# Kernel tuning notes

Measured on AMD Instinct MI355X. Metric: run time of the kernel, lower is better.

## Reference

```python
import jax, jax.numpy as jnp
import numpy as np


def _pair_indices(field_num):
    # upper-triangular (row < col) pairs, same order as the torch double loop
    r, c = np.triu_indices(field_num, k=1)
    return jnp.asarray(r, dtype=jnp.int32), jnp.asarray(c, dtype=jnp.int32)


def setup_inputs() -> dict:
    key = jax.random.key(0)
    x = jax.random.normal(key, (4096, 39, 64), dtype=jnp.float32)
    return {"x": x}


def reference(x) -> jnp.ndarray:
    # x: (B, F, D). Output: (B, F*(F-1)/2) pairwise inner products.
    field_num = x.shape[1]
    rows, cols = _pair_indices(field_num)  # static: derived from shape
    p = x[:, rows, :]  # (B, P, D) gather of row-field embeddings
    q = x[:, cols, :]  # (B, P, D) gather of col-field embeddings
    return jnp.sum(p * q, axis=2)  # (B, P)
```

## Files before the change

### kernel.cpp

```cpp
#include <hip/hip_runtime.h>


typedef __bf16 bf16x8 __attribute__((ext_vector_type(8)));
typedef float  f32x4  __attribute__((ext_vector_type(4)));

constexpr int NFIELD = 39;
constexpr int DIM    = 64;
constexpr int NPAIR  = 741;
constexpr int BPB    = 4;

__global__ __launch_bounds__(256)
void ip_kernel(const float* __restrict__ x, float* __restrict__ out, int batches) {
    __shared__ __align__(16) float lds_out[BPB][NPAIR];

    const int tid  = threadIdx.x;
    const int wv   = tid >> 6;
    const int lane = tid & 63;
    const int b0   = blockIdx.x * BPB;
    const int batch = b0 + wv;
    const int nb_here = (batches - b0) < BPB ? (batches - b0) : BPB;

    if (batch < batches) {
        const int m = lane & 15;
        const int q = lane >> 4;
        const float* xb = x + (size_t)batch * (NFIELD * DIM);

        bf16x8 fr[3][2];
        #pragma unroll
        for (int t = 0; t < 3; ++t) {
            int row = 16 * t + m;
            if (row >= NFIELD) row = NFIELD - 1;
            #pragma unroll
            for (int s = 0; s < 2; ++s) {
                const float* p = xb + row * DIM + 32 * s + 8 * q;
                f32x4 u = *(const f32x4*)p;
                f32x4 v = *(const f32x4*)(p + 4);
                bf16x8 w;
                w[0] = (__bf16)u[0]; w[1] = (__bf16)u[1];
                w[2] = (__bf16)u[2]; w[3] = (__bf16)u[3];
                w[4] = (__bf16)v[0]; w[5] = (__bf16)v[1];
                w[6] = (__bf16)v[2]; w[7] = (__bf16)v[3];
                fr[t][s] = w;
            }
        }

        f32x4 a00 = {0.f,0.f,0.f,0.f}, a01 = a00, a02 = a00;
        f32x4 a11 = a00, a12 = a00, a22 = a00;
        #pragma unroll
        for (int s = 0; s < 2; ++s) {
            a00 = __builtin_amdgcn_mfma_f32_16x16x32_bf16(fr[0][s], fr[0][s], a00, 0, 0, 0);
            a01 = __builtin_amdgcn_mfma_f32_16x16x32_bf16(fr[0][s], fr[1][s], a01, 0, 0, 0);
            a02 = __builtin_amdgcn_mfma_f32_16x16x32_bf16(fr[0][s], fr[2][s], a02, 0, 0, 0);
            a11 = __builtin_amdgcn_mfma_f32_16x16x32_bf16(fr[1][s], fr[1][s], a11, 0, 0, 0);
            a12 = __builtin_amdgcn_mfma_f32_16x16x32_bf16(fr[1][s], fr[2][s], a12, 0, 0, 0);
            a22 = __builtin_amdgcn_mfma_f32_16x16x32_bf16(fr[2][s], fr[2][s], a22, 0, 0, 0);
        }

        auto scatter = [&](const f32x4& a, int ti, int tj) {
            #pragma unroll
            for (int r = 0; r < 4; ++r) {
                const int i = 16 * ti + 4 * q + r;
                const int j = 16 * tj + m;
                if (i < j && j < NFIELD) {
                    const int p = 38 * i - (i * (i - 1)) / 2 + (j - i - 1);
                    lds_out[wv][p] = a[r];
                }
            }
        };
        scatter(a00, 0, 0); scatter(a01, 0, 1); scatter(a02, 0, 2);
        scatter(a11, 1, 1); scatter(a12, 1, 2); scatter(a22, 2, 2);
    }
    __syncthreads();

    float* dst = out + (size_t)b0 * NPAIR;
    const float* srcf = &lds_out[0][0];
    if (nb_here == BPB) {
        const float4* s4 = (const float4*)srcf;
        float4* d4 = (float4*)dst;
        for (int i = tid; i < (BPB * NPAIR) / 4; i += 256) d4[i] = s4[i];
    } else {
        const int nfl = nb_here * NPAIR;
        for (int i = tid; i < nfl; i += 256) dst[i] = srcf[i];
    }
}

extern "C" void kernel_launch(void* const* d_in, const int* in_sizes, int n_in,
                              void* d_out, int out_size, void* d_ws, size_t ws_size,
                              hipStream_t stream) {
    const float* x = (const float*)d_in[0];
    float* out     = (float*)d_out;
    const int batches = in_sizes[0] / (NFIELD * DIM);
    const int blocks  = (batches + BPB - 1) / BPB;
    ip_kernel<<<blocks, 256, 0, stream>>>(x, out, batches);
}
```

Before: 79.61 us.

## Split each batch's pair tiles across two waves and drop block barrier

Each batch is now handled by two waves instead of one. One wave computes the tile-0 row blocks and the other computes the remaining tiles. Each wave writes its own contiguous range of output pairs from LDS, so the block-wide barrier is replaced by a local lgkmcnt wait. The scatter becomes branchless, with masked elements redirected to padding slots, and the launch bounds add an occupancy hint. The intent is more parallelism and less synchronization latency, at the cost of loading tiles 1 and 2 twice and replacing float4 output stores with scalar ones.

```diff
diff --git a/kernel.cpp b/kernel.cpp
--- a/kernel.cpp
+++ b/kernel.cpp
@@ -4,84 +4,96 @@
 typedef __bf16 bf16x8 __attribute__((ext_vector_type(8)));
 typedef float  f32x4  __attribute__((ext_vector_type(4)));
 
-constexpr int NFIELD = 39;
-constexpr int DIM    = 64;
-constexpr int NPAIR  = 741;
-constexpr int BPB    = 4;
+constexpr int NFIELD    = 39;
+constexpr int DIM       = 64;
+constexpr int NPAIR     = 741;
+constexpr int BPB       = 2;
+constexpr int ROWSTRIDE = 768;
+constexpr int PSPLIT    = 488;
 
-__global__ __launch_bounds__(256)
+__global__ __launch_bounds__(256, 8)
 void ip_kernel(const float* __restrict__ x, float* __restrict__ out, int batches) {
-    __shared__ __align__(16) float lds_out[BPB][NPAIR];
+    __shared__ __align__(16) float lds_out[BPB][ROWSTRIDE];
 
     const int tid  = threadIdx.x;
     const int wv   = tid >> 6;
     const int lane = tid & 63;
+    const int role = wv & 1;
     const int b0   = blockIdx.x * BPB;
-    const int batch = b0 + wv;
-    const int nb_here = (batches - b0) < BPB ? (batches - b0) : BPB;
+    const int batch = b0 + (wv >> 1);
+    if (batch >= batches) return;
 
-    if (batch < batches) {
-        const int m = lane & 15;
-        const int q = lane >> 4;
-        const float* xb = x + (size_t)batch * (NFIELD * DIM);
+    const int m = lane & 15;
+    const int q = lane >> 4;
+    const float* xb = x + (size_t)batch * (NFIELD * DIM);
+    float* ldsrow = &lds_out[wv >> 1][0];
 
-        bf16x8 fr[3][2];
-        #pragma unroll
-        for (int t = 0; t < 3; ++t) {
-            int row = 16 * t + m;
-            if (row >= NFIELD) row = NFIELD - 1;
-            #pragma unroll
-            for (int s = 0; s < 2; ++s) {
-                const float* p = xb + row * DIM + 32 * s + 8 * q;
-                f32x4 u = *(const f32x4*)p;
-                f32x4 v = *(const f32x4*)(p + 4);
-                bf16x8 w;
-                w[0] = (__bf16)u[0]; w[1] = (__bf16)u[1];
-                w[2] = (__bf16)u[2]; w[3] = (__bf16)u[3];
-                w[4] = (__bf16)v[0]; w[5] = (__bf16)v[1];
-                w[6] = (__bf16)v[2]; w[7] = (__bf16)v[3];
-                fr[t][s] = w;
-            }
-        }
-
-        f32x4 a00 = {0.f,0.f,0.f,0.f}, a01 = a00, a02 = a00;
-        f32x4 a11 = a00, a12 = a00, a22 = a00;
+    auto loadfrag = [&](int t, bf16x8 fr[2]) {
+        int row = 16 * t + m;
+        if (row >= NFIELD) row = NFIELD - 1;
         #pragma unroll
         for (int s = 0; s < 2; ++s) {
-            a00 = __builtin_amdgcn_mfma_f32_16x16x32_bf16(fr[0][s], fr[0][s], a00, 0, 0, 0);
-            a01 = __builtin_amdgcn_mfma_f32_16x16x32_bf16(fr[0][s], fr[1][s], a01, 0, 0, 0);
-            a02 = __builtin_amdgcn_mfma_f32_16x16x32_bf16(fr[0][s], fr[2][s], a02, 0, 0, 0);
-            a11 = __builtin_amdgcn_mfma_f32_16x16x32_bf16(fr[1][s], fr[1][s], a11, 0, 0, 0);
-            a12 = __builtin_amdgcn_mfma_f32_16x16x32_bf16(fr[1][s], fr[2][s], a12, 0, 0, 0);
-            a22 = __builtin_amdgcn_mfma_f32_16x16x32_bf16(fr[2][s], fr[2][s], a22, 0, 0, 0);
+            const float* p = xb + row * DIM + 32 * s + 8 * q;
+            f32x4 u = *(const f32x4*)p;
+            f32x4 v = *(const f32x4*)(p + 4);
+            bf16x8 w;
+            w[0] = (__bf16)u[0]; w[1] = (__bf16)u[1];
+            w[2] = (__bf16)u[2]; w[3] = (__bf16)u[3];
+            w[4] = (__bf16)v[0]; w[5] = (__bf16)v[1];
+            w[6] = (__bf16)v[2]; w[7] = (__bf16)v[3];
+            fr[s] = w;
         }
+    };
 
-        auto scatter = [&](const f32x4& a, int ti, int tj) {
-            #pragma unroll
-            for (int r = 0; r < 4; ++r) {
-                const int i = 16 * ti + 4 * q + r;
-                const int j = 16 * tj + m;
-                if (i < j && j < NFIELD) {
-                    const int p = 38 * i - (i * (i - 1)) / 2 + (j - i - 1);
-                    lds_out[wv][p] = a[r];
-                }
-            }
-        };
-        scatter(a00, 0, 0); scatter(a01, 0, 1); scatter(a02, 0, 2);
-        scatter(a11, 1, 1); scatter(a12, 1, 2); scatter(a22, 2, 2);
+    auto scatter = [&](const f32x4& a, int ti, int tj, bool diag, bool jclip) {
+        int i = 16 * ti + 4 * q;
+        const int j = 16 * tj + m;
+        int base = 37 * i - (i * (i - 1)) / 2 - 1;
+        #pragma unroll
+        for (int r = 0; r < 4; ++r) {
+            bool ok = (!diag || (i < j)) && (!jclip || (j < NFIELD));
+            int p = ok ? (base + j) : (744 + (role << 3) + r);
+            ldsrow[p] = a[r];
+            base += 37 - i; ++i;
+        }
+    };
+
+    bf16x8 f1[2], f2[2];
+    loadfrag(1, f1);
+    loadfrag(2, f2);
+
+    f32x4 acc0 = {0.f,0.f,0.f,0.f}, acc1 = acc0, acc2 = acc0;
+
+    if (role == 0) {
+        bf16x8 f0[2];
+        loadfrag(0, f0);
+        #pragma unroll
+        for (int s = 0; s < 2; ++s) {
+            acc0 = __builtin_amdgcn_mfma_f32_16x16x32_bf16(f0[s], f0[s], acc0, 0, 0, 0);
+            acc1 = __builtin_amdgcn_mfma_f32_16x16x32_bf16(f0[s], f1[s], acc1, 0, 0, 0);
+            acc2 = __builtin_amdgcn_mfma_f32_16x16x32_bf16(f0[s], f2[s], acc2, 0, 0, 0);
+        }
+        scatter(acc0, 0, 0, true,  false);
+        scatter(acc1, 0, 1, false, false);
+        scatter(acc2, 0, 2, false, true);
+    } else {
+        #pragma unroll
+        for (int s = 0; s < 2; ++s) {
+            acc0 = __builtin_amdgcn_mfma_f32_16x16x32_bf16(f1[s], f1[s], acc0, 0, 0, 0);
+            acc1 = __builtin_amdgcn_mfma_f32_16x16x32_bf16(f1[s], f2[s], acc1, 0, 0, 0);
+            acc2 = __builtin_amdgcn_mfma_f32_16x16x32_bf16(f2[s], f2[s], acc2, 0, 0, 0);
+        }
+        scatter(acc0, 1, 1, true,  false);
+        scatter(acc1, 1, 2, false, true);
+        scatter(acc2, 2, 2, true,  true);
     }
-    __syncthreads();
 
-    float* dst = out + (size_t)b0 * NPAIR;
-    const float* srcf = &lds_out[0][0];
-    if (nb_here == BPB) {
-        const float4* s4 = (const float4*)srcf;
-        float4* d4 = (float4*)dst;
-        for (int i = tid; i < (BPB * NPAIR) / 4; i += 256) d4[i] = s4[i];
-    } else {
-        const int nfl = nb_here * NPAIR;
-        for (int i = tid; i < nfl; i += 256) dst[i] = srcf[i];
-    }
+    asm volatile("s_waitcnt lgkmcnt(0)" ::: "memory");
+
+    float* dst = out + (size_t)batch * NPAIR;
+    const int lo = role ? PSPLIT : 0;
+    const int hi = role ? NPAIR  : PSPLIT;
+    for (int i = lo + lane; i < hi; i += 64) dst[i] = ldsrow[i];
 }
 
 extern "C" void kernel_launch(void* const* d_in, const int* in_sizes, int n_in,
```

Result: slower. 81.29 us (+2.1%).
